# Kernel optimization log

Measured on AMD Instinct MI355X. Metric: run time of the kernel, lower is better.

Reference implementation:

```python
import jax, jax.numpy as jnp
import numpy as np
from jax import lax

COMMITMENT_COST = 0.25
NUM_EMB = 512
LATENT = 32


def _conv(x, w, b):
    # Conv2d(kernel=4, stride=2, padding=1), NCHW / OIHW
    y = lax.conv_general_dilated(x, w, window_strides=(2, 2),
                                 padding=((1, 1), (1, 1)),
                                 dimension_numbers=('NCHW', 'OIHW', 'NCHW'))
    return y + b[None, :, None, None]


def _deconv(x, w, b):
    # ConvTranspose2d(kernel=4, stride=2, padding=1); torch weight is [in, out, kh, kw].
    # Equivalent: input-dilated conv with flipped kernel, padding = k-1-p = 2.
    wf = jnp.flip(w, (2, 3)).transpose(1, 0, 2, 3)  # -> OIHW
    y = lax.conv_general_dilated(x, wf, window_strides=(1, 1),
                                 padding=((2, 2), (2, 2)),
                                 lhs_dilation=(2, 2),
                                 dimension_numbers=('NCHW', 'OIHW', 'NCHW'))
    return y + b[None, :, None, None]


def _vq(z, emb):
    # z: [B, C, H, W] -> NHWC
    zp = jnp.transpose(z, (0, 2, 3, 1))          # [B,H,W,C]
    flat = zp.reshape(-1, LATENT)                # [N,C]
    d = (jnp.sum(flat * flat, axis=1, keepdims=True)
         + jnp.sum(emb * emb, axis=1)
         - 2.0 * flat @ emb.T)                   # [N,K]
    idx = jnp.argmin(d, axis=1)                  # [N]
    q = emb[idx].reshape(zp.shape)               # gather == one_hot @ emb
    e_loss = jnp.mean((lax.stop_gradient(q) - zp) ** 2)
    q_loss = jnp.mean((q - lax.stop_gradient(zp)) ** 2)
    vq_loss = q_loss + COMMITMENT_COST * e_loss
    q_st = zp + lax.stop_gradient(q - zp)        # straight-through
    return jnp.transpose(q_st, (0, 3, 1, 2)), vq_loss, idx


def setup_inputs() -> dict:
    key = jax.random.key(0)
    ks = jax.random.split(key, 16)
    s = 0.05
    inp = {
        'x':  jax.random.uniform(ks[0], (128, 3, 128, 128), jnp.float32),
        'w1': jax.random.normal(ks[1], (32, 3, 4, 4), jnp.float32) * s,
        'b1': jax.random.normal(ks[2], (32,), jnp.float32) * s,
        'w2': jax.random.normal(ks[3], (64, 32, 4, 4), jnp.float32) * s,
        'b2': jax.random.normal(ks[4], (64,), jnp.float32) * s,
        'w3': jax.random.normal(ks[5], (LATENT, 64, 4, 4), jnp.float32) * s,
        'b3': jax.random.normal(ks[6], (LATENT,), jnp.float32) * s,
        'emb': jax.random.uniform(ks[7], (NUM_EMB, LATENT), jnp.float32,
                                  minval=-1.0 / NUM_EMB, maxval=1.0 / NUM_EMB),
        'd1': jax.random.normal(ks[8], (LATENT, 64, 4, 4), jnp.float32) * s,
        'db1': jax.random.normal(ks[9], (64,), jnp.float32) * s,
        'd2': jax.random.normal(ks[10], (64, 32, 4, 4), jnp.float32) * s,
        'db2': jax.random.normal(ks[11], (32,), jnp.float32) * s,
        'd3': jax.random.normal(ks[12], (32, 3, 4, 4), jnp.float32) * s,
        'db3': jax.random.normal(ks[13], (3,), jnp.float32) * s,
    }
    return inp


def reference(x, w1, b1, w2, b2, w3, b3, emb, d1, db1, d2, db2, d3, db3):
    # encoder
    h = jax.nn.relu(_conv(x, w1, b1))
    h = jax.nn.relu(_conv(h, w2, b2))
    z = _conv(h, w3, b3)                 # [B, LATENT, 16, 16]
    # vector quantization
    z_q, vq_loss, _ = _vq(z, emb)
    # decoder
    g = jax.nn.relu(_deconv(z_q, d1, db1))
    g = jax.nn.relu(_deconv(g, d2, db2))
    x_recon = jax.nn.sigmoid(_deconv(g, d3, db3))
    recon_loss = jnp.mean((x_recon - x) ** 2)
    return x_recon, recon_loss, vq_loss
```

## Files before the change

### kernel.cpp

```cpp
#include <hip/hip_runtime.h>
#include <math.h>

#define NEMB 512
#define LAT 32

typedef unsigned short u16;
typedef unsigned int u32;
typedef __attribute__((ext_vector_type(8))) short bf16x8;
typedef __attribute__((ext_vector_type(4))) float f32x4;

__device__ __forceinline__ u16 f2b(float f) {
    unsigned u = __builtin_bit_cast(unsigned, f);
    return (u16)((u + 0x7fffu + ((u >> 16) & 1u)) >> 16);
}
__device__ __forceinline__ float b2f(u16 h) {
    unsigned u = ((unsigned)h) << 16;
    return __builtin_bit_cast(float, u);
}
__device__ __forceinline__ void dot2(float& acc, u32 a, u32 b) {
    asm("v_dot2_f32_bf16 %0, %1, %2, %0" : "+v"(acc) : "v"(a), "v"(b));
}

union V16 { uint4 u; u16 s[8]; };
union V8  { uint2 u; u16 s[4]; };

static const size_t OFF_H1  = 0;
static const size_t OFF_H2  = 33554432;
static const size_t OFF_Z   = 50331648;
static const size_t OFF_ZQ  = 52428800;
static const size_t OFF_W2T = 54525952;
static const size_t OFF_W3T = 54591488;
static const size_t OFF_D1T = 54657024;
static const size_t OFF_D2T = 54722560;
static const size_t OFF_ACC = 54804480;
static const size_t OFF_E2  = 54808576;
static const size_t OFF_W1T = 54810624;
static const size_t OFF_XB  = 54814720;
static const size_t OFF_D3P = 72120320;

__global__ __launch_bounds__(256)
void prep_xb(const float* __restrict__ w2, const float* __restrict__ w3,
             const float* __restrict__ d1, const float* __restrict__ d2,
             const float* __restrict__ d3, const float* __restrict__ emb,
             const float* __restrict__ w1, const float* __restrict__ x,
             u16* __restrict__ w2t, u16* __restrict__ w3t, u16* __restrict__ d1t,
             u16* __restrict__ d2t, u32* __restrict__ d3p, u16* __restrict__ w1t,
             u16* __restrict__ xb,
             float* __restrict__ accum, float* __restrict__ e2) {
    if (blockIdx.x >= 528) {
        int t = (blockIdx.x - 528) * 256 + threadIdx.x;
        int xx = t % 130; int t2 = t / 130;
        int yy = t2 % 130; int n = t2 / 130;
        V8 o; o.u = (uint2){0, 0};
        if (xx >= 1 && xx <= 128 && yy >= 1 && yy <= 128) {
            size_t base = ((size_t)n * 3) * 16384 + (size_t)(yy - 1) * 128 + (xx - 1);
            o.s[0] = f2b(x[base]);
            o.s[1] = f2b(x[base + 16384]);
            o.s[2] = f2b(x[base + 32768]);
        }
        *(uint2*)&xb[(size_t)t * 4] = o.u;
        return;
    }
    int t = blockIdx.x * 256 + threadIdx.x;
    if (t < 32768) {
        int ci = t & 31; int t2 = t >> 5; int co = t2 & 63; int tau = t2 >> 6;
        w2t[t] = f2b(w2[((size_t)co * 32 + ci) * 16 + tau]);
    } else if (t < 65536) {
        int u = t - 32768;
        int ci = u & 63; int t2 = u >> 6; int co = t2 & 31; int tau = t2 >> 5;
        w3t[u] = f2b(w3[((size_t)co * 64 + ci) * 16 + tau]);
    } else if (t < 98304) {
        int u = t - 65536;
        int ci = u & 31; int t2 = u >> 5; int co = t2 & 63; int s = t2 >> 6;
        int ry = (s >> 3) & 1, rx = (s >> 2) & 1, a = (s >> 1) & 1, b = s & 1;
        int ky = ((ry + 1) & 1) + 2 * a, kx = ((rx + 1) & 1) + 2 * b;
        d1t[u] = f2b(d1[((size_t)ci * 64 + co) * 16 + ky * 4 + kx]);
    } else if (t < 131072) {
        int u = t - 98304;
        int ci = u & 63; int t2 = u >> 6; int co = t2 & 31; int s = t2 >> 5;
        int ry = (s >> 3) & 1, rx = (s >> 2) & 1, a = (s >> 1) & 1, b = s & 1;
        int ky = ((ry + 1) & 1) + 2 * a, kx = ((rx + 1) & 1) + 2 * b;
        d2t[u] = f2b(d2[((size_t)ci * 32 + co) * 16 + ky * 4 + kx]);
    } else if (t < 131584) {
        int u = t - 131072;
        float s = 0.f;
        #pragma unroll
        for (int c = 0; c < LAT; ++c) { float e = emb[u * LAT + c]; s = fmaf(e, e, s); }
        e2[u] = s;
    } else if (t < 132096) {
        accum[t - 131584] = 0.f;
    } else if (t < 134144) {
        int u = t - 132096;
        int k = u & 31; int co = (u >> 5) & 31; int c = u >> 10;
        int kyl = k >> 4, kx = (k >> 2) & 3, ch = k & 3;
        w1t[u] = (ch < 3) ? f2b(w1[((size_t)(co * 3 + ch) * 4 + (2 * c + kyl)) * 4 + kx])
                          : (u16)0;
    } else if (t < 134912) {
        int u = t - 134144;
        int kk = u & 15; int t2 = u >> 4;
        int co = t2 % 3; int cp = t2 / 3;
        u16 lo = f2b(d3[((size_t)(2 * cp) * 3 + co) * 16 + kk]);
        u16 hi = f2b(d3[((size_t)(2 * cp + 1) * 3 + co) * 16 + kk]);
        d3p[u] = (u32)lo | ((u32)hi << 16);
    }
}

__global__ __launch_bounds__(256)
void conv1_mfma(const u16* __restrict__ xb, const u16* __restrict__ w1t,
                const float* __restrict__ b1, u16* __restrict__ h1) {
    int bid = blockIdx.x;
    const int oyb = bid & 15; const int n = bid >> 4;
    const int tid = threadIdx.x, w = tid >> 6, lane = tid & 63;
    const int l15 = lane & 15, l4 = lane >> 4;
    const int oy = oyb * 4 + w;

    bf16x8 bf[2][2];
    #pragma unroll
    for (int c = 0; c < 2; ++c)
        #pragma unroll
        for (int cf = 0; cf < 2; ++cf)
            bf[c][cf] = *(const bf16x8*)&w1t[((size_t)(c * 32 + cf * 16 + l15)) * 32 + l4 * 8];

    f32x4 acc[4][2];
    #pragma unroll
    for (int f = 0; f < 4; ++f)
        #pragma unroll
        for (int cf = 0; cf < 2; ++cf) {
            float bv = b1[cf * 16 + l15];
            acc[f][cf] = (f32x4){bv, bv, bv, bv};
        }

    #pragma unroll
    for (int c = 0; c < 2; ++c) {
        const int row = 2 * oy + 2 * c + (l4 >> 1);
        #pragma unroll
        for (int f = 0; f < 4; ++f) {
            const int col = 2 * (f * 16 + l15) + (l4 & 1) * 2;
            bf16x8 a = *(const bf16x8*)&xb[(((size_t)n * 130 + row) * 130 + col) * 4];
            acc[f][0] = __builtin_amdgcn_mfma_f32_16x16x32_bf16(a, bf[c][0], acc[f][0], 0, 0, 0);
            acc[f][1] = __builtin_amdgcn_mfma_f32_16x16x32_bf16(a, bf[c][1], acc[f][1], 0, 0, 0);
        }
    }

    #pragma unroll
    for (int f = 0; f < 4; ++f)
        #pragma unroll
        for (int cf = 0; cf < 2; ++cf)
            #pragma unroll
            for (int rg = 0; rg < 4; ++rg) {
                int ox = f * 16 + l4 * 4 + rg;
                h1[(((size_t)n * 64 + oy) * 64 + ox) * 32 + cf * 16 + l15] =
                    f2b(fmaxf(acc[f][cf][rg], 0.f));
            }
}

template <int CI, int CO, int HI, int WI, bool RELU>
__global__ __launch_bounds__(256)
void mfma_conv(const u16* __restrict__ xin, const u16* __restrict__ wt,
               const float* __restrict__ bias, u16* __restrict__ out) {
    constexpr int HO = HI / 2, WO = WI / 2;
    constexpr int BCOLS = (WO < 32) ? WO : 32;
    constexpr int XC = 2 * BCOLS + 2;
    constexpr int NCOLF = BCOLS / 16, NCOF = CO / 16, NCC = CI / 32;
    constexpr int CPU8 = CI / 8;
    __shared__ u16 sx[10 * XC * CI];

    int bid = blockIdx.x;
    constexpr int NBY = HO / 4, NTX = WO / BCOLS;
    const int tx = bid % NTX; bid /= NTX;
    const int by = bid % NBY; const int n = bid / NBY;
    const int oy0 = by * 4, ox0 = tx * BCOLS;
    const int tid = threadIdx.x, w = tid >> 6, lane = tid & 63;
    const int l15 = lane & 15, l4 = lane >> 4;

    const int iyb = 2 * oy0 - 1, ixb = 2 * ox0 - 1;
    for (int u = tid; u < 10 * XC * CPU8; u += 256) {
        int c8 = u % CPU8; int t2 = u / CPU8;
        int xc = t2 % XC; int r = t2 / XC;
        int iy = iyb + r, ix = ixb + xc;
        uint4 v = {0, 0, 0, 0};
        if (iy >= 0 && iy < HI && ix >= 0 && ix < WI)
            v = *(const uint4*)&xin[(((size_t)n * HI + iy) * WI + ix) * CI + c8 * 8];
        int byte = ((r * XC + xc) * CI + c8 * 8) * 2;
        byte ^= ((xc >> 1) & 7) << 4;
        *(uint4*)&sx[byte >> 1] = v;
    }
    __syncthreads();

    f32x4 acc[NCOLF][NCOF];
    #pragma unroll
    for (int pf = 0; pf < NCOLF; ++pf)
        #pragma unroll
        for (int cf = 0; cf < NCOF; ++cf) {
            float bv = bias[cf * 16 + l15];
            acc[pf][cf] = (f32x4){bv, bv, bv, bv};
        }

    #pragma unroll 4
    for (int tau = 0; tau < 16; ++tau) {
        const int ky = tau >> 2, kx = tau & 3;
        const int r = 2 * w + ky;
        #pragma unroll
        for (int cc = 0; cc < NCC; ++cc) {
            bf16x8 b[NCOF];
            #pragma unroll
            for (int cf = 0; cf < NCOF; ++cf)
                b[cf] = *(const bf16x8*)&wt[((size_t)(tau * CO + cf * 16 + l15)) * CI + cc * 32 + l4 * 8];
            bf16x8 a[NCOLF];
            #pragma unroll
            for (int pf = 0; pf < NCOLF; ++pf) {
                int xc = 2 * (pf * 16 + l15) + kx;
                int byte = ((r * XC + xc) * CI + cc * 32 + l4 * 8) * 2;
                byte ^= ((xc >> 1) & 7) << 4;
                a[pf] = *(const bf16x8*)&sx[byte >> 1];
            }
            #pragma unroll
            for (int pf = 0; pf < NCOLF; ++pf)
                #pragma unroll
                for (int cf = 0; cf < NCOF; ++cf)
                    acc[pf][cf] = __builtin_amdgcn_mfma_f32_16x16x32_bf16(
                        a[pf], b[cf], acc[pf][cf], 0, 0, 0);
        }
    }

    const int oy = oy0 + w;
    #pragma unroll
    for (int pf = 0; pf < NCOLF; ++pf)
        #pragma unroll
        for (int cf = 0; cf < NCOF; ++cf)
            #pragma unroll
            for (int rg = 0; rg < 4; ++rg) {
                int ox = ox0 + pf * 16 + l4 * 4 + rg;
                float v = acc[pf][cf][rg];
                if (RELU) v = fmaxf(v, 0.f);
                out[(((size_t)n * HO + oy) * WO + ox) * CO + cf * 16 + l15] = f2b(v);
            }
}

template <int CI, int CO, int HI, int WI>
__global__ __launch_bounds__(256)
void mfma_deconv_wl(const u16* __restrict__ xin, const u16* __restrict__ wt,
                    const float* __restrict__ bias, u16* __restrict__ out) {
    constexpr int HO = 2 * HI, WO = 2 * WI;
    constexpr int BCOLS = (WI < 32) ? WI : 32;
    constexpr int XC = BCOLS + 2;
    constexpr int NCOLF = BCOLS / 16, NCOF = CO / 16, NCC = CI / 32;
    constexpr int CPU8 = CI / 8;
    __shared__ u16 sx[5 * XC * CI];
    __shared__ u16 swt[8 * CO * CI];

    const int ry = blockIdx.y;
    int bid = blockIdx.x;
    constexpr int NBY = HI / 4, NTX = WI / BCOLS;
    const int tx = bid % NTX; bid /= NTX;
    const int by = bid % NBY; const int n = bid / NBY;
    const int q0 = by * 4, r0 = tx * BCOLS;
    const int tid = threadIdx.x, w = tid >> 6, lane = tid & 63;
    const int l15 = lane & 15, l4 = lane >> 4;

    const int qb = q0 + ry - 1;
    for (int u = tid; u < 5 * XC * CPU8; u += 256) {
        int c8 = u % CPU8; int t2 = u / CPU8;
        int xc = t2 % XC; int r = t2 / XC;
        int iy = qb + r, ix = r0 - 1 + xc;
        uint4 v = {0, 0, 0, 0};
        if (iy >= 0 && iy < HI && ix >= 0 && ix < WI)
            v = *(const uint4*)&xin[(((size_t)n * HI + iy) * WI + ix) * CI + c8 * 8];
        int byte = ((r * XC + xc) * CI + c8 * 8) * 2;
        byte ^= (xc & 7) << 4;
        *(uint4*)&sx[byte >> 1] = v;
    }
    const u16* wts = wt + (size_t)(ry * 8) * CO * CI;
    for (int u = tid; u < 8 * CO * CPU8; u += 256) {
        int c8 = u % CPU8; int t2 = u / CPU8;
        int co = t2 % CO; int l = t2 / CO;
        uint4 v = *(const uint4*)&wts[((size_t)l * CO + co) * CI + c8 * 8];
        int byte = ((l * CO + co) * CI + c8 * 8) * 2;
        byte ^= (co & 7) << 4;
        *(uint4*)&swt[byte >> 1] = v;
    }
    __syncthreads();

    f32x4 acc[2][NCOLF][NCOF];
    #pragma unroll
    for (int rx = 0; rx < 2; ++rx)
        #pragma unroll
        for (int pf = 0; pf < NCOLF; ++pf)
            #pragma unroll
            for (int cf = 0; cf < NCOF; ++cf) {
                float bv = bias[cf * 16 + l15];
                acc[rx][pf][cf] = (f32x4){bv, bv, bv, bv};
            }

    #pragma unroll
    for (int rx = 0; rx < 2; ++rx) {
        #pragma unroll
        for (int tap = 0; tap < 4; ++tap) {
            const int a_ = tap >> 1, b_ = tap & 1;
            const int r = w + 1 - a_;
            const int l = rx * 4 + tap;
            #pragma unroll
            for (int cc = 0; cc < NCC; ++cc) {
                bf16x8 b[NCOF];
                #pragma unroll
                for (int cf = 0; cf < NCOF; ++cf) {
                    int co = cf * 16 + l15;
                    int byte = (((l * CO + co) * CI + cc * 32 + l4 * 8) * 2) ^ ((co & 7) << 4);
                    b[cf] = *(const bf16x8*)((const char*)swt + byte);
                }
                bf16x8 a[NCOLF];
                #pragma unroll
                for (int pf = 0; pf < NCOLF; ++pf) {
                    int xc = pf * 16 + l15 + rx - b_ + 1;
                    int byte = ((r * XC + xc) * CI + cc * 32 + l4 * 8) * 2;
                    byte ^= (xc & 7) << 4;
                    a[pf] = *(const bf16x8*)&sx[byte >> 1];
                }
                #pragma unroll
                for (int pf = 0; pf < NCOLF; ++pf)
                    #pragma unroll
                    for (int cf = 0; cf < NCOF; ++cf)
                        acc[rx][pf][cf] = __builtin_amdgcn_mfma_f32_16x16x32_bf16(
                            a[pf], b[cf], acc[rx][pf][cf], 0, 0, 0);
            }
        }
    }

    const int oy = 2 * (q0 + w) + ry;
    #pragma unroll
    for (int rx = 0; rx < 2; ++rx)
        #pragma unroll
        for (int pf = 0; pf < NCOLF; ++pf)
            #pragma unroll
            for (int cf = 0; cf < NCOF; ++cf)
                #pragma unroll
                for (int rg = 0; rg < 4; ++rg) {
                    int ox = 2 * (r0 + pf * 16 + l4 * 4 + rg) + rx;
                    float v = fmaxf(acc[rx][pf][cf][rg], 0.f);
                    out[(((size_t)n * HO + oy) * WO + ox) * CO + cf * 16 + l15] = f2b(v);
                }
}

__global__ __launch_bounds__(256)
void deconv3_dot2(const u16* __restrict__ g2, const u32* __restrict__ d3p,
                  const float* __restrict__ db3, float* __restrict__ out,
                  const float* __restrict__ ref, float* __restrict__ buckets) {
    __shared__ u32 sxp[16 * 412];
    __shared__ u32 sw[768];
    int bid = blockIdx.x;
    const int ty = bid & 15; const int n = bid >> 4;
    const int tid = threadIdx.x;
    const int w = tid >> 6, lane = tid & 63;
    const int row = (w & 1) + 4 * (w >> 1) + 2 * (lane >> 5);
    const int cg = lane & 31;

    const int iy_org = ty * 4 - 1;

    for (int u = tid; u < 6 * 66 * 4; u += 256) {
        int c8 = u & 3; int pos = u >> 2;
        int col = pos % 66; int r = pos / 66;
        int iy = iy_org + r, ix = col - 1;
        uint4 v = {0, 0, 0, 0};
        if (iy >= 0 && iy < 64 && ix >= 0 && ix < 64)
            v = *(const uint4*)&g2[(((size_t)n * 64 + iy) * 64 + ix) * 32 + c8 * 8];
        int base = r * 68 + col;
        sxp[(c8 * 4 + 0) * 412 + base] = v.x;
        sxp[(c8 * 4 + 1) * 412 + base] = v.y;
        sxp[(c8 * 4 + 2) * 412 + base] = v.z;
        sxp[(c8 * 4 + 3) * 412 + base] = v.w;
    }
    for (int l = tid; l < 768; l += 256) sw[l] = d3p[l];
    __syncthreads();

    const int ky0 = (row + 1) & 1;
    const int iyA = ((row + 1 - ky0) >> 1) + 1;
    const int iyB = iyA - 1;
    const int q = cg * 2;

    float acc[3][4];
    #pragma unroll
    for (int co = 0; co < 3; ++co) {
        float b = db3[co];
        #pragma unroll
        for (int p = 0; p < 4; ++p) acc[co][p] = b;
    }

    #pragma unroll 1
    for (int c2 = 0; c2 < 16; ++c2) {
        uint4 hA = *(const uint4*)&sxp[c2 * 412 + iyA * 68 + q];
        uint4 hB = *(const uint4*)&sxp[c2 * 412 + iyB * 68 + q];
        u32 ta[4] = {hA.x, hA.y, hA.z, hA.w};
        u32 tb[4] = {hB.x, hB.y, hB.z, hB.w};
        #pragma unroll
        for (int co = 0; co < 3; ++co) {
            uint4 wA = *(const uint4*)&sw[(c2 * 3 + co) * 16 + ky0 * 4];
            uint4 wB = *(const uint4*)&sw[(c2 * 3 + co) * 16 + (ky0 + 2) * 4];
            #pragma unroll
            for (int p = 0; p < 4; ++p) {
                const int A = (p + 3) >> 1;
                const int B = (p + 1) >> 1;
                if (((p + 1) & 1) == 1) {
                    dot2(acc[co][p], ta[A], wA.y);
                    dot2(acc[co][p], ta[B], wA.w);
                    dot2(acc[co][p], tb[A], wB.y);
                    dot2(acc[co][p], tb[B], wB.w);
                } else {
                    dot2(acc[co][p], ta[A], wA.x);
                    dot2(acc[co][p], ta[B], wA.z);
                    dot2(acc[co][p], tb[A], wB.x);
                    dot2(acc[co][p], tb[B], wB.z);
                }
            }
        }
    }

    const int oy = ty * 8 + row, oxb = cg * 4;
    float lsum = 0.f;
    #pragma unroll
    for (int co = 0; co < 3; ++co) {
        size_t oi = (((size_t)n * 3 + co) * 128 + oy) * 128 + oxb;
        float4 rf = *(const float4*)&ref[oi];
        float4 st;
        st.x = 1.f / (1.f + __expf(-acc[co][0]));
        st.y = 1.f / (1.f + __expf(-acc[co][1]));
        st.z = 1.f / (1.f + __expf(-acc[co][2]));
        st.w = 1.f / (1.f + __expf(-acc[co][3]));
        *(float4*)&out[oi] = st;
        float d0 = st.x - rf.x, d1 = st.y - rf.y, d2 = st.z - rf.z, d3v = st.w - rf.w;
        lsum += d0 * d0 + d1 * d1 + d2 * d2 + d3v * d3v;
    }
    #pragma unroll
    for (int off = 32; off; off >>= 1) lsum += __shfl_down(lsum, off, 64);
    if ((tid & 63) == 0) atomicAdd(&buckets[blockIdx.x & 255], lsum);
}

__global__ __launch_bounds__(256)
void vq_mfma(const u16* __restrict__ z, const float* __restrict__ emb,
             const float* __restrict__ e2g, u16* __restrict__ zq,
             float* __restrict__ vq_buckets) {
    __shared__ u16 semb[NEMB * LAT];
    __shared__ float se2[NEMB];
    const int tid = threadIdx.x;

    for (int u = tid; u < 2048; u += 256) {
        int code = u >> 2, seg = u & 3;
        const float4* ep = (const float4*)&emb[code * 32 + seg * 8];
        float4 e0 = ep[0], e1 = ep[1];
        V16 o;
        o.s[0] = f2b(e0.x); o.s[1] = f2b(e0.y); o.s[2] = f2b(e0.z); o.s[3] = f2b(e0.w);
        o.s[4] = f2b(e1.x); o.s[5] = f2b(e1.y); o.s[6] = f2b(e1.z); o.s[7] = f2b(e1.w);
        int byte = (code * 64 + seg * 16) ^ ((code & 7) << 4);
        *(uint4*)((char*)semb + byte) = o.u;
    }
    if (tid < NEMB) se2[tid] = e2g[tid];
    __syncthreads();

    const int w = tid >> 6, lane = tid & 63;
    const int l15 = lane & 15, l4 = lane >> 4;
    const int rowbase = blockIdx.x * 64 + w * 16;

    bf16x8 a = *(const bf16x8*)&z[(size_t)(rowbase + l15) * LAT + l4 * 8];

    float best[4] = {1e30f, 1e30f, 1e30f, 1e30f};
    int   bidx[4] = {0, 0, 0, 0};
    #pragma unroll
    for (int f = 0; f < 32; ++f) {
        int byteb = ((f * 16 + l15) * 64 + l4 * 16) ^ ((l15 & 7) << 4);
        bf16x8 bfrag = *(const bf16x8*)((const char*)semb + byteb);
        f32x4 s = {0.f, 0.f, 0.f, 0.f};
        s = __builtin_amdgcn_mfma_f32_16x16x32_bf16(a, bfrag, s, 0, 0, 0);
        float e2c = se2[f * 16 + l15];
        int cidx = f * 16 + l15;
        #pragma unroll
        for (int j = 0; j < 4; ++j) {
            float d = fmaf(s[j], -2.f, e2c);
            bool lt = d < best[j];
            best[j] = lt ? d : best[j];
            bidx[j] = lt ? cidx : bidx[j];
        }
    }
    #pragma unroll
    for (int m = 1; m < 16; m <<= 1) {
        #pragma unroll
        for (int j = 0; j < 4; ++j) {
            float ob = __shfl_xor(best[j], m, 64);
            int   oi = __shfl_xor(bidx[j], m, 64);
            bool take = (ob < best[j]) || (ob == best[j] && oi < bidx[j]);
            best[j] = take ? ob : best[j];
            bidx[j] = take ? oi : bidx[j];
        }
    }
    const int r = lane >> 2;
    const int j0 = r & 3;
    int k = (j0 == 0) ? bidx[0] : (j0 == 1) ? bidx[1] : (j0 == 2) ? bidx[2] : bidx[3];
    const int seg = lane & 3;
    const float4* ep = (const float4*)&emb[k * LAT + seg * 8];
    float4 e0 = ep[0], e1 = ep[1];
    float ev[8] = {e0.x, e0.y, e0.z, e0.w, e1.x, e1.y, e1.z, e1.w};
    size_t zoff = (size_t)(rowbase + r) * LAT + seg * 8;
    V16 zr; zr.u = *(const uint4*)&z[zoff];
    V16 o;
    float local = 0.f;
    #pragma unroll
    for (int jj = 0; jj < 8; ++jj) {
        float dd = ev[jj] - b2f(zr.s[jj]);
        local = fmaf(dd, dd, local);
        o.s[jj] = f2b(ev[jj]);
    }
    *(uint4*)&zq[zoff] = o.u;
    #pragma unroll
    for (int off = 32; off; off >>= 1) local += __shfl_down(local, off, 64);
    if (lane == 0) atomicAdd(&vq_buckets[blockIdx.x & 255], local);
}

__global__ void finalize_kernel(const float* __restrict__ accum, float* __restrict__ out,
                                int out_size) {
    int tid = threadIdx.x;
    float v  = accum[tid];
    float vq = accum[256 + tid];
    #pragma unroll
    for (int off = 32; off; off >>= 1) {
        v  += __shfl_down(v, off, 64);
        vq += __shfl_down(vq, off, 64);
    }
    __shared__ float s[8];
    if ((tid & 63) == 0) { s[tid >> 6] = v; s[4 + (tid >> 6)] = vq; }
    __syncthreads();
    if (tid == 0) {
        float rt = s[0] + s[1] + s[2] + s[3];
        float qt = s[4] + s[5] + s[6] + s[7];
        out[out_size - 2] = rt / 6291456.f;
        out[out_size - 1] = 1.25f * qt / 1048576.f;
    }
}

extern "C" void kernel_launch(void* const* d_in, const int* in_sizes, int n_in,
                              void* d_out, int out_size, void* d_ws, size_t ws_size,
                              hipStream_t stream) {
    const float* x   = (const float*)d_in[0];
    const float* w1  = (const float*)d_in[1];
    const float* b1  = (const float*)d_in[2];
    const float* w2  = (const float*)d_in[3];
    const float* b2  = (const float*)d_in[4];
    const float* w3  = (const float*)d_in[5];
    const float* b3  = (const float*)d_in[6];
    const float* emb = (const float*)d_in[7];
    const float* d1  = (const float*)d_in[8];
    const float* db1 = (const float*)d_in[9];
    const float* d2  = (const float*)d_in[10];
    const float* db2 = (const float*)d_in[11];
    const float* d3  = (const float*)d_in[12];
    const float* db3 = (const float*)d_in[13];

    char* ws = (char*)d_ws;
    u16* h1  = (u16*)(ws + OFF_H1);
    u16* h2  = (u16*)(ws + OFF_H2);
    u16* zb  = (u16*)(ws + OFF_Z);
    u16* zqb = (u16*)(ws + OFF_ZQ);
    u16* w2t = (u16*)(ws + OFF_W2T);
    u16* w3t = (u16*)(ws + OFF_W3T);
    u16* d1t = (u16*)(ws + OFF_D1T);
    u16* d2t = (u16*)(ws + OFF_D2T);
    u32* d3p = (u32*)(ws + OFF_D3P);
    u16* w1t = (u16*)(ws + OFF_W1T);
    u16* xb  = (u16*)(ws + OFF_XB);
    float* acc = (float*)(ws + OFF_ACC);
    float* e2  = (float*)(ws + OFF_E2);
    float* out = (float*)d_out;

    prep_xb<<<528 + 8450, 256, 0, stream>>>(w2, w3, d1, d2, d3, emb, w1, x,
                                            w2t, w3t, d1t, d2t, d3p, w1t, xb, acc, e2);

    conv1_mfma<<<2048, 256, 0, stream>>>(xb, w1t, b1, h1);
    mfma_conv<32, 64, 64, 64, true ><<<1024, 256, 0, stream>>>(h1, w2t, b2, h2);
    mfma_conv<64, 32, 32, 32, false><<<512, 256, 0, stream>>>(h2, w3t, b3, zb);

    vq_mfma<<<512, 256, 0, stream>>>(zb, emb, e2, zqb, acc + 256);

    u16* g1 = h2; u16* g2 = h1;
    mfma_deconv_wl<32, 64, 16, 16><<<dim3(512, 2), 256, 0, stream>>>(zqb, d1t, db1, g1);
    mfma_deconv_wl<64, 32, 32, 32><<<dim3(1024, 2), 256, 0, stream>>>(g1, d2t, db2, g2);
    deconv3_dot2<<<2048, 256, 0, stream>>>(g2, d3p, db3, out, x, acc);

    finalize_kernel<<<1, 256, 0, stream>>>(acc, out, out_size);
}
```

Measured before the change: 155.7 us.

## Fuse conv3 encoder layer with vector quantization in one kernel

Replaces the separate conv3 and VQ kernels with one kernel. Each block computes a 4x16 tile of latent vectors in registers via MFMA, stages them in LDS, then reuses the same LDS (aliased) to hold the bf16 codebook for the nearest-code search. This removes one launch and the global round trip of the z tensor. In exchange every block reconverts the full codebook, and LDS use rises to about 43KB, which may limit occupancy.

Result: no change. 157.6 us (+1.2%).

```diff
diff --git a/kernel.cpp b/kernel.cpp
--- a/kernel.cpp
+++ b/kernel.cpp
@@ -26,7 +26,6 @@
 
 static const size_t OFF_H1  = 0;
 static const size_t OFF_H2  = 33554432;
-static const size_t OFF_Z   = 50331648;
 static const size_t OFF_ZQ  = 52428800;
 static const size_t OFF_W2T = 54525952;
 static const size_t OFF_W3T = 54591488;
@@ -237,6 +236,136 @@
             }
 }
 
+__global__ __launch_bounds__(256)
+void conv3_vq(const u16* __restrict__ xin, const u16* __restrict__ wt,
+              const float* __restrict__ bias, const float* __restrict__ emb,
+              const float* __restrict__ e2g, u16* __restrict__ zq,
+              float* __restrict__ vq_buckets) {
+    __shared__ char smem[43520];
+    u16*   sx   = (u16*)smem;
+    u16*   semb = (u16*)smem;
+    float* se2  = (float*)(smem + 32768);
+    u16*   zt   = (u16*)(smem + 34816);
+
+    int bid = blockIdx.x;
+    const int by = bid & 3; const int n = bid >> 2;
+    const int oy0 = by * 4;
+    const int tid = threadIdx.x, w = tid >> 6, lane = tid & 63;
+    const int l15 = lane & 15, l4 = lane >> 4;
+
+    const int iyb = 2 * oy0 - 1;
+    for (int u = tid; u < 10 * 34 * 8; u += 256) {
+        int c8 = u % 8; int t2 = u / 8;
+        int xc = t2 % 34; int r = t2 / 34;
+        int iy = iyb + r, ix = xc - 1;
+        uint4 v = {0, 0, 0, 0};
+        if (iy >= 0 && iy < 32 && ix >= 0 && ix < 32)
+            v = *(const uint4*)&xin[(((size_t)n * 32 + iy) * 32 + ix) * 64 + c8 * 8];
+        int byte = ((r * 34 + xc) * 64 + c8 * 8) * 2;
+        byte ^= ((xc >> 1) & 7) << 4;
+        *(uint4*)&sx[byte >> 1] = v;
+    }
+    __syncthreads();
+
+    f32x4 acc[2];
+    #pragma unroll
+    for (int cf = 0; cf < 2; ++cf) {
+        float bv = bias[cf * 16 + l15];
+        acc[cf] = (f32x4){bv, bv, bv, bv};
+    }
+
+    #pragma unroll 4
+    for (int tau = 0; tau < 16; ++tau) {
+        const int ky = tau >> 2, kx = tau & 3;
+        const int r = 2 * w + ky;
+        #pragma unroll
+        for (int cc = 0; cc < 2; ++cc) {
+            bf16x8 b[2];
+            #pragma unroll
+            for (int cf = 0; cf < 2; ++cf)
+                b[cf] = *(const bf16x8*)&wt[((size_t)(tau * 32 + cf * 16 + l15)) * 64 + cc * 32 + l4 * 8];
+            int xc = 2 * l15 + kx;
+            int byte = ((r * 34 + xc) * 64 + cc * 32 + l4 * 8) * 2;
+            byte ^= ((xc >> 1) & 7) << 4;
+            bf16x8 a = *(const bf16x8*)&sx[byte >> 1];
+            acc[0] = __builtin_amdgcn_mfma_f32_16x16x32_bf16(a, b[0], acc[0], 0, 0, 0);
+            acc[1] = __builtin_amdgcn_mfma_f32_16x16x32_bf16(a, b[1], acc[1], 0, 0, 0);
+        }
+    }
+    __syncthreads();
+
+    for (int u = tid; u < 2048; u += 256) {
+        int code = u >> 2, seg = u & 3;
+        const float4* ep = (const float4*)&emb[code * 32 + seg * 8];
+        float4 e0 = ep[0], e1 = ep[1];
+        V16 o;
+        o.s[0] = f2b(e0.x); o.s[1] = f2b(e0.y); o.s[2] = f2b(e0.z); o.s[3] = f2b(e0.w);
+        o.s[4] = f2b(e1.x); o.s[5] = f2b(e1.y); o.s[6] = f2b(e1.z); o.s[7] = f2b(e1.w);
+        int byte = (code * 64 + seg * 16) ^ ((code & 7) << 4);
+        *(uint4*)((char*)semb + byte) = o.u;
+    }
+    for (int u = tid; u < NEMB; u += 256) se2[u] = e2g[u];
+    #pragma unroll
+    for (int cf = 0; cf < 2; ++cf)
+        #pragma unroll
+        for (int rg = 0; rg < 4; ++rg)
+            zt[(w * 16 + l4 * 4 + rg) * 40 + cf * 16 + l15] = f2b(acc[cf][rg]);
+    __syncthreads();
+
+    bf16x8 a = *(const bf16x8*)&zt[(w * 16 + l15) * 40 + l4 * 8];
+
+    float best[4] = {1e30f, 1e30f, 1e30f, 1e30f};
+    int   bidx[4] = {0, 0, 0, 0};
+    #pragma unroll
+    for (int f = 0; f < 32; ++f) {
+        int byteb = ((f * 16 + l15) * 64 + l4 * 16) ^ ((l15 & 7) << 4);
+        bf16x8 bfrag = *(const bf16x8*)((const char*)semb + byteb);
+        f32x4 s = {0.f, 0.f, 0.f, 0.f};
+        s = __builtin_amdgcn_mfma_f32_16x16x32_bf16(a, bfrag, s, 0, 0, 0);
+        float e2c = se2[f * 16 + l15];
+        int cidx = f * 16 + l15;
+        #pragma unroll
+        for (int j = 0; j < 4; ++j) {
+            float d = fmaf(s[j], -2.f, e2c);
+            bool lt = d < best[j];
+            best[j] = lt ? d : best[j];
+            bidx[j] = lt ? cidx : bidx[j];
+        }
+    }
+    #pragma unroll
+    for (int m = 1; m < 16; m <<= 1) {
+        #pragma unroll
+        for (int j = 0; j < 4; ++j) {
+            float ob = __shfl_xor(best[j], m, 64);
+            int   oi = __shfl_xor(bidx[j], m, 64);
+            bool take = (ob < best[j]) || (ob == best[j] && oi < bidx[j]);
+            best[j] = take ? ob : best[j];
+            bidx[j] = take ? oi : bidx[j];
+        }
+    }
+    const int r = lane >> 2;
+    const int j0 = r & 3;
+    int k = (j0 == 0) ? bidx[0] : (j0 == 1) ? bidx[1] : (j0 == 2) ? bidx[2] : bidx[3];
+    const int seg = lane & 3;
+    const float4* ep = (const float4*)&emb[k * LAT + seg * 8];
+    float4 e0 = ep[0], e1 = ep[1];
+    float ev[8] = {e0.x, e0.y, e0.z, e0.w, e1.x, e1.y, e1.z, e1.w};
+    V16 zr; zr.u = *(const uint4*)&zt[(w * 16 + r) * 40 + seg * 8];
+    size_t zoff = ((size_t)n * 256 + (size_t)(oy0 + w) * 16 + r) * LAT + seg * 8;
+    V16 o;
+    float local = 0.f;
+    #pragma unroll
+    for (int jj = 0; jj < 8; ++jj) {
+        float dd = ev[jj] - b2f(zr.s[jj]);
+        local = fmaf(dd, dd, local);
+        o.s[jj] = f2b(ev[jj]);
+    }
+    *(uint4*)&zq[zoff] = o.u;
+    #pragma unroll
+    for (int off = 32; off; off >>= 1) local += __shfl_down(local, off, 64);
+    if (lane == 0) atomicAdd(&vq_buckets[blockIdx.x & 255], local);
+}
+
 template <int CI, int CO, int HI, int WI>
 __global__ __launch_bounds__(256)
 void mfma_deconv_wl(const u16* __restrict__ xin, const u16* __restrict__ wt,
@@ -434,85 +563,6 @@
     if ((tid & 63) == 0) atomicAdd(&buckets[blockIdx.x & 255], lsum);
 }
 
-__global__ __launch_bounds__(256)
-void vq_mfma(const u16* __restrict__ z, const float* __restrict__ emb,
-             const float* __restrict__ e2g, u16* __restrict__ zq,
-             float* __restrict__ vq_buckets) {
-    __shared__ u16 semb[NEMB * LAT];
-    __shared__ float se2[NEMB];
-    const int tid = threadIdx.x;
-
-    for (int u = tid; u < 2048; u += 256) {
-        int code = u >> 2, seg = u & 3;
-        const float4* ep = (const float4*)&emb[code * 32 + seg * 8];
-        float4 e0 = ep[0], e1 = ep[1];
-        V16 o;
-        o.s[0] = f2b(e0.x); o.s[1] = f2b(e0.y); o.s[2] = f2b(e0.z); o.s[3] = f2b(e0.w);
-        o.s[4] = f2b(e1.x); o.s[5] = f2b(e1.y); o.s[6] = f2b(e1.z); o.s[7] = f2b(e1.w);
-        int byte = (code * 64 + seg * 16) ^ ((code & 7) << 4);
-        *(uint4*)((char*)semb + byte) = o.u;
-    }
-    if (tid < NEMB) se2[tid] = e2g[tid];
-    __syncthreads();
-
-    const int w = tid >> 6, lane = tid & 63;
-    const int l15 = lane & 15, l4 = lane >> 4;
-    const int rowbase = blockIdx.x * 64 + w * 16;
-
-    bf16x8 a = *(const bf16x8*)&z[(size_t)(rowbase + l15) * LAT + l4 * 8];
-
-    float best[4] = {1e30f, 1e30f, 1e30f, 1e30f};
-    int   bidx[4] = {0, 0, 0, 0};
-    #pragma unroll
-    for (int f = 0; f < 32; ++f) {
-        int byteb = ((f * 16 + l15) * 64 + l4 * 16) ^ ((l15 & 7) << 4);
-        bf16x8 bfrag = *(const bf16x8*)((const char*)semb + byteb);
-        f32x4 s = {0.f, 0.f, 0.f, 0.f};
-        s = __builtin_amdgcn_mfma_f32_16x16x32_bf16(a, bfrag, s, 0, 0, 0);
-        float e2c = se2[f * 16 + l15];
-        int cidx = f * 16 + l15;
-        #pragma unroll
-        for (int j = 0; j < 4; ++j) {
-            float d = fmaf(s[j], -2.f, e2c);
-            bool lt = d < best[j];
-            best[j] = lt ? d : best[j];
-            bidx[j] = lt ? cidx : bidx[j];
-        }
-    }
-    #pragma unroll
-    for (int m = 1; m < 16; m <<= 1) {
-        #pragma unroll
-        for (int j = 0; j < 4; ++j) {
-            float ob = __shfl_xor(best[j], m, 64);
-            int   oi = __shfl_xor(bidx[j], m, 64);
-            bool take = (ob < best[j]) || (ob == best[j] && oi < bidx[j]);
-            best[j] = take ? ob : best[j];
-            bidx[j] = take ? oi : bidx[j];
-        }
-    }
-    const int r = lane >> 2;
-    const int j0 = r & 3;
-    int k = (j0 == 0) ? bidx[0] : (j0 == 1) ? bidx[1] : (j0 == 2) ? bidx[2] : bidx[3];
-    const int seg = lane & 3;
-    const float4* ep = (const float4*)&emb[k * LAT + seg * 8];
-    float4 e0 = ep[0], e1 = ep[1];
-    float ev[8] = {e0.x, e0.y, e0.z, e0.w, e1.x, e1.y, e1.z, e1.w};
-    size_t zoff = (size_t)(rowbase + r) * LAT + seg * 8;
-    V16 zr; zr.u = *(const uint4*)&z[zoff];
-    V16 o;
-    float local = 0.f;
-    #pragma unroll
-    for (int jj = 0; jj < 8; ++jj) {
-        float dd = ev[jj] - b2f(zr.s[jj]);
-        local = fmaf(dd, dd, local);
-        o.s[jj] = f2b(ev[jj]);
-    }
-    *(uint4*)&zq[zoff] = o.u;
-    #pragma unroll
-    for (int off = 32; off; off >>= 1) local += __shfl_down(local, off, 64);
-    if (lane == 0) atomicAdd(&vq_buckets[blockIdx.x & 255], local);
-}
-
 __global__ void finalize_kernel(const float* __restrict__ accum, float* __restrict__ out,
                                 int out_size) {
     int tid = threadIdx.x;
@@ -555,7 +605,6 @@
     char* ws = (char*)d_ws;
     u16* h1  = (u16*)(ws + OFF_H1);
     u16* h2  = (u16*)(ws + OFF_H2);
-    u16* zb  = (u16*)(ws + OFF_Z);
     u16* zqb = (u16*)(ws + OFF_ZQ);
     u16* w2t = (u16*)(ws + OFF_W2T);
     u16* w3t = (u16*)(ws + OFF_W3T);
@@ -573,9 +622,8 @@
 
     conv1_mfma<<<2048, 256, 0, stream>>>(xb, w1t, b1, h1);
     mfma_conv<32, 64, 64, 64, true ><<<1024, 256, 0, stream>>>(h1, w2t, b2, h2);
-    mfma_conv<64, 32, 32, 32, false><<<512, 256, 0, stream>>>(h2, w3t, b3, zb);
-
-    vq_mfma<<<512, 256, 0, stream>>>(zb, emb, e2, zqb, acc + 256);
+
+    conv3_vq<<<512, 256, 0, stream>>>(h2, w3t, b3, emb, e2, zqb, acc + 256);
 
     u16* g1 = h2; u16* g2 = h1;
     mfma_deconv_wl<32, 64, 16, 16><<<dim3(512, 2), 256, 0, stream>>>(zqb, d1t, db1, g1);
```
